# Optimization experiments

Measured on AMD Instinct MI355X. Metric: run time of the kernel, lower is better.

The kernel has to match this reference:

```python
import jax, jax.numpy as jnp
import numpy as np

NUM_FEAT = 10

def _flatten(x):
    # [B,T,C,H,W] -> [B,C,T*H*W]
    B, T, C, H, W = x.shape
    return jnp.transpose(x, (0, 2, 1, 3, 4)).reshape(B, C, T * H * W)

def _conv1x1(w, b, x):
    # pointwise Conv1d: w [F,C], b [F], x [B,C,N] -> [B,F,N]
    return jnp.einsum('fc,bcn->bfn', w, x) + b[None, :, None]

def setup_inputs() -> dict:
    key = jax.random.key(0)
    ks = jax.random.split(key, 9)
    B, T, C, H, W = 1, 5, 64, 32, 32
    F = NUM_FEAT
    return {
        'input1': jax.random.normal(ks[0], (B, T, C, H, W), jnp.float32),
        'input2': jax.random.normal(ks[1], (B, T, C, H, W), jnp.float32),
        'act_weights': jax.random.uniform(ks[2], (3,), jnp.float32),
        'conv1_w': jax.random.normal(ks[3], (F, C), jnp.float32) * 0.05,
        'conv1_b': jnp.zeros((F,), jnp.float32),
        'conv2_w': jax.random.normal(ks[4], (F, C), jnp.float32) * 0.05,
        'conv2_b': jnp.zeros((F,), jnp.float32),
        'g3_w': jax.random.normal(ks[5], (F, C), jnp.float32) * 0.05,
        'g3_b': jnp.zeros((F,), jnp.float32),
    }

def reference(input1, input2, act_weights, conv1_w, conv1_b, conv2_w, conv2_b, g3_w, g3_b):
    B, T, C, H, W = input1.shape
    F = conv1_w.shape[0]
    x1 = _flatten(input1)                    # [B,C,N]
    x2 = _flatten(input2)                    # [B,C,N]
    q = _conv1x1(conv1_w, conv1_b, x1)       # [B,F,N]
    k = _conv1x1(conv2_w, conv2_b, x2)       # [B,F,N]
    v = _conv1x1(g3_w, g3_b, x1)             # [B,F,N]
    scores = jnp.einsum('bfn,bfm->bnm', q, k)  # [B,N,N] (same math, computed once)

    def branch(act_scores):
        o = jnp.einsum('bnm,bfm->bnf', act_scores, v)      # [B,N,F]
        o = o.reshape(B, T, H, W, F)
        return jnp.transpose(o, (0, 1, 4, 2, 3))           # [B,T,F,H,W]

    out = act_weights[0] * branch(jax.nn.relu(scores))
    out = out + act_weights[1] * branch(jax.nn.sigmoid(scores))
    # NOTE: original code scales the softmax branch by act_weights[0] (bug kept faithfully)
    out = out + act_weights[0] * branch(jax.nn.softmax(scores, axis=1))
    return out
```

## Files before the change

### kernel.cpp

```cpp
#include <hip/hip_runtime.h>

#define N_TOK   5120
#define C_IN    64
#define F_OUT   10
#define FP      12

#define DTILE   40
#define MTILE   40
#define NCHUNKS 128
#define MCHUNKS 128


__global__ __launch_bounds__(256) void qkv_kernel(
    const float* __restrict__ x1, const float* __restrict__ x2,
    const float* __restrict__ w1, const float* __restrict__ b1,
    const float* __restrict__ w2, const float* __restrict__ b2,
    const float* __restrict__ w3, const float* __restrict__ b3,
    float* __restrict__ Q, float* __restrict__ K, float* __restrict__ V,
    float* __restrict__ out, float* __restrict__ dsum)
{
    if (blockIdx.x < 200)
        out[blockIdx.x * 256 + threadIdx.x] = 0.f;
    else if (blockIdx.x < 220)
        dsum[(blockIdx.x - 200) * 256 + threadIdx.x] = 0.f;

    int arr = blockIdx.x / 200;
    int rem = blockIdx.x - arr * 200;
    int f   = rem / 20;
    int nbk = rem - f * 20;
    int n   = nbk * 256 + threadIdx.x;
    int t = n >> 10, p = n & 1023;

    const float* x    = (arr == 1) ? x2 : x1;
    const float* w    = (arr == 0) ? w1 : (arr == 1) ? w2 : w3;
    const float* bias = (arr == 0) ? b1 : (arr == 1) ? b2 : b3;
    float*       dst  = (arr == 0) ? Q  : (arr == 1) ? K  : V;

    const float* xp = x + t * (C_IN * 1024) + p;
    const float* wr = w + f * C_IN;

    float4 wv[16];
#pragma unroll
    for (int i = 0; i < 16; ++i) wv[i] = ((const float4*)wr)[i];

    float acc = 0.f;
#pragma unroll
    for (int i = 0; i < 16; ++i) {
        acc = fmaf(wv[i].x, xp[(4 * i + 0) * 1024], acc);
        acc = fmaf(wv[i].y, xp[(4 * i + 1) * 1024], acc);
        acc = fmaf(wv[i].z, xp[(4 * i + 2) * 1024], acc);
        acc = fmaf(wv[i].w, xp[(4 * i + 3) * 1024], acc);
    }
    dst[n * FP + f] = acc + bias[f];
}

__global__ __launch_bounds__(256) void denom_kernel(
    const float* __restrict__ Q, const float* __restrict__ K,
    float* __restrict__ dsum, int nclen)
{
    int mTile = blockIdx.x % 20;
    int nc    = blockIdx.x / 20;
    int tid   = threadIdx.x;
    int m0 = mTile * 256 + tid;

    float kk[10];
    {
        const float* kp = K + m0 * FP;
        float4 a = ((const float4*)kp)[0];
        float4 b = ((const float4*)kp)[1];
        float2 e = ((const float2*)kp)[4];
        kk[0]=a.x; kk[1]=a.y; kk[2]=a.z; kk[3]=a.w;
        kk[4]=b.x; kk[5]=b.y; kk[6]=b.z; kk[7]=b.w;
        kk[8]=e.x; kk[9]=e.y;
    }

    __shared__ __align__(16) float sq[DTILE * FP];

    float d = 0.f;
    int n0 = nc * nclen;
    for (int base = n0; base < n0 + nclen; base += DTILE) {
        __syncthreads();
        if (tid < DTILE * FP / 4)
            ((float4*)sq)[tid] = ((const float4*)(Q + base * FP))[tid];
        __syncthreads();
#pragma unroll 4
        for (int j = 0; j < DTILE; ++j) {
            const float4* qp = (const float4*)(sq + j * FP);
            float4 qa = qp[0], qb = qp[1], qc = qp[2];
            float s0 = 0.f, s1 = 0.f;
            s0 = fmaf(qa.x, kk[0], s0);  s1 = fmaf(qb.y, kk[5], s1);
            s0 = fmaf(qa.y, kk[1], s0);  s1 = fmaf(qb.z, kk[6], s1);
            s0 = fmaf(qa.z, kk[2], s0);  s1 = fmaf(qb.w, kk[7], s1);
            s0 = fmaf(qa.w, kk[3], s0);  s1 = fmaf(qc.x, kk[8], s1);
            s0 = fmaf(qb.x, kk[4], s0);  s1 = fmaf(qc.y, kk[9], s1);
            d += __expf(fminf(s0 + s1, 60.f));
        }
    }
    atomicAdd(&dsum[m0], d);
}

__global__ __launch_bounds__(256) void main_kernel(
    const float* __restrict__ Q, const float* __restrict__ K,
    const float* __restrict__ V, const float* __restrict__ dsum,
    const float* __restrict__ aw, float* __restrict__ out, int mclen)
{
    int nTile = blockIdx.x % 20;
    int mc    = blockIdx.x / 20;
    int tid   = threadIdx.x;
    int nb = nTile * 256 + tid;
    float w0 = aw[0], w1v = aw[1];

    float q[10];
    {
        const float* qp = Q + nb * FP;
        float4 a = ((const float4*)qp)[0];
        float4 b = ((const float4*)qp)[1];
        float2 e = ((const float2*)qp)[4];
        q[0]=a.x; q[1]=a.y; q[2]=a.z; q[3]=a.w;
        q[4]=b.x; q[5]=b.y; q[6]=b.z; q[7]=b.w;
        q[8]=e.x; q[9]=e.y;
    }

    float acc[F_OUT];
#pragma unroll
    for (int f = 0; f < F_OUT; ++f) acc[f] = 0.f;

    __shared__ __align__(16) float sk[MTILE * FP];
    __shared__ __align__(16) float sv[MTILE * FP];
    __shared__ float siw[MTILE];

    int mstart = mc * mclen;
    for (int mbase = mstart; mbase < mstart + mclen; mbase += MTILE) {
        __syncthreads();
        if (tid < 120)
            ((float4*)sk)[tid] = ((const float4*)(K + mbase * FP))[tid];
        else if (tid < 240)
            ((float4*)sv)[tid - 120] = ((const float4*)(V + mbase * FP))[tid - 120];
        if (tid < MTILE)
            siw[tid] = w0 * __builtin_amdgcn_rcpf(dsum[mbase + tid]);
        __syncthreads();

#pragma unroll 4
        for (int j = 0; j < MTILE; ++j) {
            const float4* kp = (const float4*)(sk + j * FP);
            float4 ka = kp[0], kb = kp[1], kc = kp[2];
            float iw = siw[j];

            float s0 = 0.f, s1 = 0.f;
            s0 = fmaf(ka.x, q[0], s0);  s1 = fmaf(kb.y, q[5], s1);
            s0 = fmaf(ka.y, q[1], s0);  s1 = fmaf(kb.z, q[6], s1);
            s0 = fmaf(ka.z, q[2], s0);  s1 = fmaf(kb.w, q[7], s1);
            s0 = fmaf(ka.w, q[3], s0);  s1 = fmaf(kc.x, q[8], s1);
            s0 = fmaf(kb.x, q[4], s0);  s1 = fmaf(kc.y, q[9], s1);
            float s  = s0 + s1;
            float rl = fmaxf(s, 0.f);
            float e  = __expf(fminf(s, 60.f));
            float sg = e * __builtin_amdgcn_rcpf(1.f + e);
            float cf = fmaf(e, iw, fmaf(w1v, sg, w0 * rl));

            const float4* vp = (const float4*)(sv + j * FP);
            float4 va = vp[0], vb4 = vp[1], vc = vp[2];
            acc[0] = fmaf(cf, va.x,  acc[0]);
            acc[1] = fmaf(cf, va.y,  acc[1]);
            acc[2] = fmaf(cf, va.z,  acc[2]);
            acc[3] = fmaf(cf, va.w,  acc[3]);
            acc[4] = fmaf(cf, vb4.x, acc[4]);
            acc[5] = fmaf(cf, vb4.y, acc[5]);
            acc[6] = fmaf(cf, vb4.z, acc[6]);
            acc[7] = fmaf(cf, vb4.w, acc[7]);
            acc[8] = fmaf(cf, vc.x,  acc[8]);
            acc[9] = fmaf(cf, vc.y,  acc[9]);
        }
    }

    int t = nb >> 10, p = nb & 1023;
    float* obase = out + ((t * F_OUT) << 10) + p;
#pragma unroll
    for (int f = 0; f < F_OUT; ++f)
        atomicAdd(obase + (f << 10), acc[f]);
}

extern "C" void kernel_launch(void* const* d_in, const int* in_sizes, int n_in,
                              void* d_out, int out_size, void* d_ws, size_t ws_size,
                              hipStream_t stream)
{
    const float* in1 = (const float*)d_in[0];
    const float* in2 = (const float*)d_in[1];
    const float* aw  = (const float*)d_in[2];
    const float* w1  = (const float*)d_in[3];
    const float* b1  = (const float*)d_in[4];
    const float* w2  = (const float*)d_in[5];
    const float* b2  = (const float*)d_in[6];
    const float* w3  = (const float*)d_in[7];
    const float* b3  = (const float*)d_in[8];
    float* out = (float*)d_out;

    float* ws   = (float*)d_ws;
    float* Q    = ws;
    float* K    = Q + N_TOK * FP;
    float* V    = K + N_TOK * FP;
    float* dsum = V + N_TOK * FP;

    int nclen = N_TOK / NCHUNKS;
    int mclen = N_TOK / MCHUNKS;

    qkv_kernel<<<600, 256, 0, stream>>>(in1, in2, w1, b1, w2, b2, w3, b3,
                                        Q, K, V, out, dsum);
    denom_kernel<<<20 * NCHUNKS, 256, 0, stream>>>(Q, K, dsum, nclen);
    main_kernel<<<20 * MCHUNKS, 256, 0, stream>>>(Q, K, V, dsum, aw, out, mclen);
}
```

Measured before the change: 117.5 us.

## Compute attention scores with packed fp16 dot2 and merge K/V/weight tiles

The Q·K score dot products in both the denominator and main kernels now use packed half-precision operands with v_dot2 (fdot2) instructions, which halves the FMA count for the scores. In the main kernel, the K (packed fp16), per-column softmax weight and V values are interleaved into a single 20-word shared-memory row, so each inner iteration issues four 16-byte LDS reads instead of separate K, V and weight loads. Tile staging now converts rows with only 40 threads. The trade-off is reduced precision in the scores, which feed an exp, so fp16 rounding of Q and K could push the output past tolerance.

```diff
diff --git a/kernel.cpp b/kernel.cpp
--- a/kernel.cpp
+++ b/kernel.cpp
@@ -10,6 +10,16 @@
 #define NCHUNKS 128
 #define MCHUNKS 128
 
+
+typedef _Float16 h2 __attribute__((ext_vector_type(2)));
+
+__device__ __forceinline__ uint pack2(float a, float b) {
+    h2 h = { (_Float16)a, (_Float16)b };
+    return __builtin_bit_cast(uint, h);
+}
+__device__ __forceinline__ h2    as_h2(uint u) { return __builtin_bit_cast(h2, u); }
+__device__ __forceinline__ float as_f(uint u)  { return __builtin_bit_cast(float, u); }
+__device__ __forceinline__ uint  as_u(float f) { return __builtin_bit_cast(uint, f); }
 
 __global__ __launch_bounds__(256) void qkv_kernel(
     const float* __restrict__ x1, const float* __restrict__ x2,
@@ -63,37 +73,46 @@
     int tid   = threadIdx.x;
     int m0 = mTile * 256 + tid;
 
-    float kk[10];
+    h2 kh[5];
     {
         const float* kp = K + m0 * FP;
         float4 a = ((const float4*)kp)[0];
         float4 b = ((const float4*)kp)[1];
         float2 e = ((const float2*)kp)[4];
-        kk[0]=a.x; kk[1]=a.y; kk[2]=a.z; kk[3]=a.w;
-        kk[4]=b.x; kk[5]=b.y; kk[6]=b.z; kk[7]=b.w;
-        kk[8]=e.x; kk[9]=e.y;
-    }
-
-    __shared__ __align__(16) float sq[DTILE * FP];
+        kh[0] = h2{ (_Float16)a.x, (_Float16)a.y };
+        kh[1] = h2{ (_Float16)a.z, (_Float16)a.w };
+        kh[2] = h2{ (_Float16)b.x, (_Float16)b.y };
+        kh[3] = h2{ (_Float16)b.z, (_Float16)b.w };
+        kh[4] = h2{ (_Float16)e.x, (_Float16)e.y };
+    }
+
+    __shared__ __align__(16) uint sq[DTILE * 12];
 
     float d = 0.f;
     int n0 = nc * nclen;
     for (int base = n0; base < n0 + nclen; base += DTILE) {
         __syncthreads();
-        if (tid < DTILE * FP / 4)
-            ((float4*)sq)[tid] = ((const float4*)(Q + base * FP))[tid];
+        if (tid < DTILE) {
+            const float* qp = Q + (base + tid) * FP;
+            float4 a = ((const float4*)qp)[0];
+            float4 b = ((const float4*)qp)[1];
+            float2 e = ((const float2*)qp)[4];
+            uint* dst = sq + tid * 12;
+            ((uint4*)dst)[0] = make_uint4(pack2(a.x, a.y), pack2(a.z, a.w),
+                                          pack2(b.x, b.y), pack2(b.z, b.w));
+            dst[4] = pack2(e.x, e.y);
+        }
         __syncthreads();
 #pragma unroll 4
         for (int j = 0; j < DTILE; ++j) {
-            const float4* qp = (const float4*)(sq + j * FP);
-            float4 qa = qp[0], qb = qp[1], qc = qp[2];
-            float s0 = 0.f, s1 = 0.f;
-            s0 = fmaf(qa.x, kk[0], s0);  s1 = fmaf(qb.y, kk[5], s1);
-            s0 = fmaf(qa.y, kk[1], s0);  s1 = fmaf(qb.z, kk[6], s1);
-            s0 = fmaf(qa.z, kk[2], s0);  s1 = fmaf(qb.w, kk[7], s1);
-            s0 = fmaf(qa.w, kk[3], s0);  s1 = fmaf(qc.x, kk[8], s1);
-            s0 = fmaf(qb.x, kk[4], s0);  s1 = fmaf(qc.y, kk[9], s1);
-            d += __expf(fminf(s0 + s1, 60.f));
+            uint4 A  = ((const uint4*)(sq + j * 12))[0];
+            uint  a4 = sq[j * 12 + 4];
+            float s = __builtin_amdgcn_fdot2(as_h2(A.x), kh[0], 0.f, false);
+            s = __builtin_amdgcn_fdot2(as_h2(A.y), kh[1], s, false);
+            s = __builtin_amdgcn_fdot2(as_h2(A.z), kh[2], s, false);
+            s = __builtin_amdgcn_fdot2(as_h2(A.w), kh[3], s, false);
+            s = __builtin_amdgcn_fdot2(as_h2(a4),  kh[4], s, false);
+            d += __expf(fminf(s, 60.f));
         }
     }
     atomicAdd(&dsum[m0], d);
@@ -110,66 +129,78 @@
     int nb = nTile * 256 + tid;
     float w0 = aw[0], w1v = aw[1];
 
-    float q[10];
+    h2 qh[5];
     {
         const float* qp = Q + nb * FP;
         float4 a = ((const float4*)qp)[0];
         float4 b = ((const float4*)qp)[1];
         float2 e = ((const float2*)qp)[4];
-        q[0]=a.x; q[1]=a.y; q[2]=a.z; q[3]=a.w;
-        q[4]=b.x; q[5]=b.y; q[6]=b.z; q[7]=b.w;
-        q[8]=e.x; q[9]=e.y;
+        qh[0] = h2{ (_Float16)a.x, (_Float16)a.y };
+        qh[1] = h2{ (_Float16)a.z, (_Float16)a.w };
+        qh[2] = h2{ (_Float16)b.x, (_Float16)b.y };
+        qh[3] = h2{ (_Float16)b.z, (_Float16)b.w };
+        qh[4] = h2{ (_Float16)e.x, (_Float16)e.y };
     }
 
     float acc[F_OUT];
 #pragma unroll
     for (int f = 0; f < F_OUT; ++f) acc[f] = 0.f;
 
-    __shared__ __align__(16) float sk[MTILE * FP];
-    __shared__ __align__(16) float sv[MTILE * FP];
-    __shared__ float siw[MTILE];
+    __shared__ __align__(16) uint sm[MTILE * 20];
 
     int mstart = mc * mclen;
     for (int mbase = mstart; mbase < mstart + mclen; mbase += MTILE) {
         __syncthreads();
-        if (tid < 120)
-            ((float4*)sk)[tid] = ((const float4*)(K + mbase * FP))[tid];
-        else if (tid < 240)
-            ((float4*)sv)[tid - 120] = ((const float4*)(V + mbase * FP))[tid - 120];
-        if (tid < MTILE)
-            siw[tid] = w0 * __builtin_amdgcn_rcpf(dsum[mbase + tid]);
+        if (tid < MTILE) {
+            int m = mbase + tid;
+            const float* kp = K + m * FP;
+            float4 ka = ((const float4*)kp)[0];
+            float4 kb = ((const float4*)kp)[1];
+            float2 kc = ((const float2*)kp)[4];
+            const float* vp = V + m * FP;
+            float4 va = ((const float4*)vp)[0];
+            float4 vb = ((const float4*)vp)[1];
+            float2 vc = ((const float2*)vp)[4];
+            float iw = w0 * __builtin_amdgcn_rcpf(dsum[m]);
+            uint* dst = sm + tid * 20;
+            ((uint4*)dst)[0] = make_uint4(pack2(ka.x, ka.y), pack2(ka.z, ka.w),
+                                          pack2(kb.x, kb.y), pack2(kb.z, kb.w));
+            ((uint4*)dst)[1] = make_uint4(pack2(kc.x, kc.y), as_u(iw),
+                                          as_u(va.x), as_u(va.y));
+            ((uint4*)dst)[2] = make_uint4(as_u(va.z), as_u(va.w),
+                                          as_u(vb.x), as_u(vb.y));
+            ((uint4*)dst)[3] = make_uint4(as_u(vb.z), as_u(vb.w),
+                                          as_u(vc.x), as_u(vc.y));
+        }
         __syncthreads();
 
 #pragma unroll 4
         for (int j = 0; j < MTILE; ++j) {
-            const float4* kp = (const float4*)(sk + j * FP);
-            float4 ka = kp[0], kb = kp[1], kc = kp[2];
-            float iw = siw[j];
-
-            float s0 = 0.f, s1 = 0.f;
-            s0 = fmaf(ka.x, q[0], s0);  s1 = fmaf(kb.y, q[5], s1);
-            s0 = fmaf(ka.y, q[1], s0);  s1 = fmaf(kb.z, q[6], s1);
-            s0 = fmaf(ka.z, q[2], s0);  s1 = fmaf(kb.w, q[7], s1);
-            s0 = fmaf(ka.w, q[3], s0);  s1 = fmaf(kc.x, q[8], s1);
-            s0 = fmaf(kb.x, q[4], s0);  s1 = fmaf(kc.y, q[9], s1);
-            float s  = s0 + s1;
+            const uint4* rp = (const uint4*)(sm + j * 20);
+            uint4 A = rp[0], B = rp[1], C = rp[2], D = rp[3];
+
+            float s = __builtin_amdgcn_fdot2(qh[0], as_h2(A.x), 0.f, false);
+            s = __builtin_amdgcn_fdot2(qh[1], as_h2(A.y), s, false);
+            s = __builtin_amdgcn_fdot2(qh[2], as_h2(A.z), s, false);
+            s = __builtin_amdgcn_fdot2(qh[3], as_h2(A.w), s, false);
+            s = __builtin_amdgcn_fdot2(qh[4], as_h2(B.x), s, false);
+
+            float iw = as_f(B.y);
             float rl = fmaxf(s, 0.f);
             float e  = __expf(fminf(s, 60.f));
             float sg = e * __builtin_amdgcn_rcpf(1.f + e);
             float cf = fmaf(e, iw, fmaf(w1v, sg, w0 * rl));
 
-            const float4* vp = (const float4*)(sv + j * FP);
-            float4 va = vp[0], vb4 = vp[1], vc = vp[2];
-            acc[0] = fmaf(cf, va.x,  acc[0]);
-            acc[1] = fmaf(cf, va.y,  acc[1]);
-            acc[2] = fmaf(cf, va.z,  acc[2]);
-            acc[3] = fmaf(cf, va.w,  acc[3]);
-            acc[4] = fmaf(cf, vb4.x, acc[4]);
-            acc[5] = fmaf(cf, vb4.y, acc[5]);
-            acc[6] = fmaf(cf, vb4.z, acc[6]);
-            acc[7] = fmaf(cf, vb4.w, acc[7]);
-            acc[8] = fmaf(cf, vc.x,  acc[8]);
-            acc[9] = fmaf(cf, vc.y,  acc[9]);
+            acc[0] = fmaf(cf, as_f(B.z), acc[0]);
+            acc[1] = fmaf(cf, as_f(B.w), acc[1]);
+            acc[2] = fmaf(cf, as_f(C.x), acc[2]);
+            acc[3] = fmaf(cf, as_f(C.y), acc[3]);
+            acc[4] = fmaf(cf, as_f(C.z), acc[4]);
+            acc[5] = fmaf(cf, as_f(C.w), acc[5]);
+            acc[6] = fmaf(cf, as_f(D.x), acc[6]);
+            acc[7] = fmaf(cf, as_f(D.y), acc[7]);
+            acc[8] = fmaf(cf, as_f(D.z), acc[8]);
+            acc[9] = fmaf(cf, as_f(D.w), acc[9]);
         }
     }
 
```

Measured after the change: 113.0 us. 3.9% less time.
